# Kernel tuning notes

Measured on AMD Instinct MI355X. Metric: run time of the kernel, lower is better.

Reference implementation:

```python
import jax, jax.numpy as jnp
import numpy as np


def setup_inputs() -> dict:
    key = jax.random.key(0)
    x = jax.random.normal(key, (4096, 16384), dtype=jnp.float32)
    return {"x": x, "k": 64}


def reference(x, k):
    # TopK activation: keep the k largest-|value| entries per row, zero the rest.
    if k <= 0:
        return jnp.zeros_like(x)
    kk = min(k, x.shape[-1])
    _, idx = jax.lax.top_k(jnp.abs(x), kk)          # idx: [rows, kk]
    rows = jnp.arange(x.shape[0])[:, None]          # [rows, 1]
    mask = jnp.zeros_like(x).at[rows, idx].set(1.0)  # scatter ones at top-k positions
    return x * mask
```

## Files before the change

kernel.cpp:

```cpp
#include <hip/hip_runtime.h>

#define ROW_LEN 16384
#define THREADS 256
#define VPT 16
#define NBINS 2048
#define CAP 1024

typedef float f4v __attribute__((ext_vector_type(4)));

__global__ __launch_bounds__(THREADS, 4)
void topk_act_kernel(const float* __restrict__ x, const int* __restrict__ kptr,
                     float* __restrict__ out)
{
    const int t = threadIdx.x;
    const long long row = blockIdx.x;
    const f4v* __restrict__ xv = (const f4v*)(x + row * ROW_LEN);
    f4v* __restrict__ ov = (f4v*)(out + row * ROW_LEN);

    const int k = *kptr;
    if (k <= 0) {
        f4v z = (f4v)(0.0f);
        #pragma unroll
        for (int j = 0; j < VPT; ++j)
            __builtin_nontemporal_store(z, &ov[j * THREADS + t]);
        return;
    }
    const unsigned kk = (unsigned)(k < ROW_LEN ? k : ROW_LEN);

    float va[VPT * 4];
    #pragma unroll
    for (int j = 0; j < VPT; ++j) {
        f4v tmp = __builtin_nontemporal_load(&xv[j * THREADS + t]);
        va[4 * j + 0] = tmp.x;
        va[4 * j + 1] = tmp.y;
        va[4 * j + 2] = tmp.z;
        va[4 * j + 3] = tmp.w;
    }

    __shared__ unsigned hist[NBINS];
    __shared__ unsigned tsum[THREADS];
    __shared__ unsigned long long lst[CAP];
    __shared__ unsigned s_cnt;
    __shared__ int s_b;
    __shared__ unsigned s_g;
    __shared__ unsigned long long s_ccut;

    for (int i = t; i < NBINS; i += THREADS) hist[i] = 0u;
    if (t == 0) s_cnt = 0u;
    __syncthreads();

    #pragma unroll
    for (int e = 0; e < VPT * 4; ++e) {
        float a = fabsf(va[e]);
        int bin = (int)(a * 512.0f);
        bin = bin > (NBINS - 1) ? (NBINS - 1) : bin;
        atomicAdd(&hist[bin], 1u);
    }
    __syncthreads();

    unsigned s = 0;
    #pragma unroll
    for (int i = 0; i < 8; ++i) s += hist[t * 8 + i];
    tsum[t] = s;
    __syncthreads();
    for (int off = 1; off < THREADS; off <<= 1) {
        unsigned add = (t + off < THREADS) ? tsum[t + off] : 0u;
        __syncthreads();
        tsum[t] += add;
        __syncthreads();
    }
    {
        unsigned acc = (t + 1 < THREADS) ? tsum[t + 1] : 0u;
        #pragma unroll
        for (int i = 7; i >= 0; --i) {
            int bin = t * 8 + i;
            unsigned h = hist[bin];
            if (acc < kk && acc + h >= kk) { s_b = bin; s_g = acc; }
            acc += h;
        }
    }
    __syncthreads();

    const int b = s_b;
    const unsigned g = s_g;

    #pragma unroll
    for (int e = 0; e < VPT * 4; ++e) {
        float a = fabsf(va[e]);
        int bin = (int)(a * 512.0f);
        bin = bin > (NBINS - 1) ? (NBINS - 1) : bin;
        if (bin == b) {
            unsigned p = atomicAdd(&s_cnt, 1u);
            if (p < CAP) {
                unsigned idx = (unsigned)((e >> 2) * (THREADS * 4) + t * 4 + (e & 3));
                lst[p] = ((unsigned long long)__float_as_uint(a) << 32)
                       | (unsigned)(~idx);
            }
        }
    }
    __syncthreads();

    const unsigned m = s_cnt < CAP ? s_cnt : CAP;
    unsigned r = kk - g;
    if (r > m) r = m;

    for (unsigned e = t; e < m; e += THREADS) {
        unsigned long long ce = lst[e];
        unsigned rank = 0;
        for (unsigned q = 0; q < m; ++q) rank += (lst[q] > ce) ? 1u : 0u;
        if (rank == r - 1) s_ccut = ce;
    }
    __syncthreads();
    const unsigned long long ccut = s_ccut;

    #pragma unroll
    for (int j = 0; j < VPT; ++j) {
        f4v w;
        #pragma unroll
        for (int c = 0; c < 4; ++c) {
            float f = va[4 * j + c];
            float a = fabsf(f);
            int bin = (int)(a * 512.0f);
            bin = bin > (NBINS - 1) ? (NBINS - 1) : bin;
            bool keep;
            if (bin > b) keep = true;
            else if (bin < b) keep = false;
            else {
                unsigned idx = (unsigned)(j * (THREADS * 4) + t * 4 + c);
                unsigned long long ce = ((unsigned long long)__float_as_uint(a) << 32)
                                      | (unsigned)(~idx);
                keep = (ce >= ccut);
            }
            w[c] = keep ? f : 0.0f;
        }
        __builtin_nontemporal_store(w, &ov[j * THREADS + t]);
    }
}

extern "C" void kernel_launch(void* const* d_in, const int* in_sizes, int n_in,
                              void* d_out, int out_size, void* d_ws, size_t ws_size,
                              hipStream_t stream) {
    const float* x  = (const float*)d_in[0];
    const int*   kp = (const int*)d_in[1];
    float* out = (float*)d_out;
    const int rows = out_size / ROW_LEN;
    topk_act_kernel<<<dim3(rows), dim3(THREADS), 0, stream>>>(x, kp, out);
}
```

Before: 543.6 us.

## Prefilter candidates above fixed threshold, rebin survivors, reload row instead of registers

Stops holding the whole row in registers. It first collects only elements with |x|>=2.0 into shared memory through a wave-ballot compaction. When enough candidates fit, it histograms just those, finds the boundary bin and ranks within that bin. Otherwise it falls back to the full histogram path, which rereads the row from global memory. The final pass reloads x and keeps every element whose key is at or above the cutoff key. This cuts register pressure and per-element shared atomics. The cost is a second global read of each row, and the fixed threshold suits normally distributed inputs.

```diff
diff --git a/kernel.cpp b/kernel.cpp
--- a/kernel.cpp
+++ b/kernel.cpp
@@ -2,17 +2,51 @@
 
 #define ROW_LEN 16384
 #define THREADS 256
-#define VPT 16
+#define ITERS (ROW_LEN / (THREADS * 4))
 #define NBINS 2048
 #define CAP 1024
+#define TPRE 2.0f
 
 typedef float f4v __attribute__((ext_vector_type(4)));
 
-__global__ __launch_bounds__(THREADS, 4)
+__device__ __forceinline__ unsigned long long make_key(float a, unsigned idx) {
+    return ((unsigned long long)__float_as_uint(a) << 32) | (unsigned)(~idx);
+}
+
+__device__ __forceinline__ void find_boundary(const unsigned* hist, unsigned kk,
+                                              int* s_b, unsigned* s_g, unsigned* wtot) {
+    const int t = threadIdx.x;
+    const int lane = t & 63;
+    const int w = t >> 6;
+    unsigned s_own = 0;
+    #pragma unroll
+    for (int i = 0; i < 8; ++i) s_own += hist[t * 8 + i];
+    unsigned acc = s_own;
+    #pragma unroll
+    for (int off = 1; off < 64; off <<= 1) {
+        unsigned v = __shfl_down(acc, off);
+        if (lane + off < 64) acc += v;
+    }
+    if (lane == 0) wtot[w] = acc;
+    __syncthreads();
+    unsigned addw = 0;
+    for (int w2 = w + 1; w2 < 4; ++w2) addw += wtot[w2];
+    unsigned above = acc - s_own + addw;
+    #pragma unroll
+    for (int i = 7; i >= 0; --i) {
+        unsigned h = hist[t * 8 + i];
+        if (above < kk && above + h >= kk) { *s_b = t * 8 + i; *s_g = above; }
+        above += h;
+    }
+    __syncthreads();
+}
+
+__global__ __launch_bounds__(THREADS)
 void topk_act_kernel(const float* __restrict__ x, const int* __restrict__ kptr,
                      float* __restrict__ out)
 {
     const int t = threadIdx.x;
+    const int lane = t & 63;
     const long long row = blockIdx.x;
     const f4v* __restrict__ xv = (const f4v*)(x + row * ROW_LEN);
     f4v* __restrict__ ov = (f4v*)(out + row * ROW_LEN);
@@ -21,119 +55,142 @@
     if (k <= 0) {
         f4v z = (f4v)(0.0f);
         #pragma unroll
-        for (int j = 0; j < VPT; ++j)
+        for (int j = 0; j < ITERS; ++j)
             __builtin_nontemporal_store(z, &ov[j * THREADS + t]);
         return;
     }
     const unsigned kk = (unsigned)(k < ROW_LEN ? k : ROW_LEN);
 
-    float va[VPT * 4];
-    #pragma unroll
-    for (int j = 0; j < VPT; ++j) {
-        f4v tmp = __builtin_nontemporal_load(&xv[j * THREADS + t]);
-        va[4 * j + 0] = tmp.x;
-        va[4 * j + 1] = tmp.y;
-        va[4 * j + 2] = tmp.z;
-        va[4 * j + 3] = tmp.w;
-    }
-
     __shared__ unsigned hist[NBINS];
-    __shared__ unsigned tsum[THREADS];
     __shared__ unsigned long long lst[CAP];
+    __shared__ unsigned wtot[4];
     __shared__ unsigned s_cnt;
     __shared__ int s_b;
     __shared__ unsigned s_g;
     __shared__ unsigned long long s_ccut;
 
-    for (int i = t; i < NBINS; i += THREADS) hist[i] = 0u;
     if (t == 0) s_cnt = 0u;
     __syncthreads();
 
-    #pragma unroll
-    for (int e = 0; e < VPT * 4; ++e) {
-        float a = fabsf(va[e]);
-        int bin = (int)(a * 512.0f);
-        bin = bin > (NBINS - 1) ? (NBINS - 1) : bin;
-        atomicAdd(&hist[bin], 1u);
-    }
-    __syncthreads();
-
-    unsigned s = 0;
-    #pragma unroll
-    for (int i = 0; i < 8; ++i) s += hist[t * 8 + i];
-    tsum[t] = s;
-    __syncthreads();
-    for (int off = 1; off < THREADS; off <<= 1) {
-        unsigned add = (t + off < THREADS) ? tsum[t + off] : 0u;
-        __syncthreads();
-        tsum[t] += add;
-        __syncthreads();
-    }
-    {
-        unsigned acc = (t + 1 < THREADS) ? tsum[t + 1] : 0u;
+    const unsigned long long lmask_lt = (1ull << lane) - 1ull;
+
+    for (int it = 0; it < ITERS; ++it) {
+        f4v v = xv[it * THREADS + t];
         #pragma unroll
-        for (int i = 7; i >= 0; --i) {
-            int bin = t * 8 + i;
-            unsigned h = hist[bin];
-            if (acc < kk && acc + h >= kk) { s_b = bin; s_g = acc; }
-            acc += h;
-        }
-    }
-    __syncthreads();
-
-    const int b = s_b;
-    const unsigned g = s_g;
-
-    #pragma unroll
-    for (int e = 0; e < VPT * 4; ++e) {
-        float a = fabsf(va[e]);
-        int bin = (int)(a * 512.0f);
-        bin = bin > (NBINS - 1) ? (NBINS - 1) : bin;
-        if (bin == b) {
-            unsigned p = atomicAdd(&s_cnt, 1u);
-            if (p < CAP) {
-                unsigned idx = (unsigned)((e >> 2) * (THREADS * 4) + t * 4 + (e & 3));
-                lst[p] = ((unsigned long long)__float_as_uint(a) << 32)
-                       | (unsigned)(~idx);
-            }
-        }
-    }
-    __syncthreads();
-
-    const unsigned m = s_cnt < CAP ? s_cnt : CAP;
-    unsigned r = kk - g;
-    if (r > m) r = m;
-
-    for (unsigned e = t; e < m; e += THREADS) {
-        unsigned long long ce = lst[e];
-        unsigned rank = 0;
-        for (unsigned q = 0; q < m; ++q) rank += (lst[q] > ce) ? 1u : 0u;
-        if (rank == r - 1) s_ccut = ce;
-    }
-    __syncthreads();
+        for (int c = 0; c < 4; ++c) {
+            float a = fabsf(v[c]);
+            bool cond = (a >= TPRE);
+            unsigned long long mk = __ballot(cond);
+            unsigned cnt = (unsigned)__popcll(mk);
+            if (cnt) {
+                unsigned base = 0;
+                if (lane == 0) base = atomicAdd(&s_cnt, cnt);
+                base = __shfl(base, 0);
+                if (cond) {
+                    unsigned pos = base + (unsigned)__popcll(mk & lmask_lt);
+                    if (pos < CAP) {
+                        unsigned idx = (unsigned)((it * THREADS + t) * 4 + c);
+                        lst[pos] = make_key(a, idx);
+                    }
+                }
+            }
+        }
+    }
+    __syncthreads();
+
+    const unsigned m_all = s_cnt;
+    const bool fast = (m_all >= kk && m_all <= CAP);
+
+    if (fast) {
+        for (int i = t; i < NBINS; i += THREADS) hist[i] = 0u;
+        __syncthreads();
+        for (unsigned e = t; e < m_all; e += THREADS) {
+            float a = __uint_as_float((unsigned)(lst[e] >> 32));
+            int rb = (int)((a - TPRE) * 1024.0f);
+            rb = rb > (NBINS - 1) ? (NBINS - 1) : rb;
+            atomicAdd(&hist[rb], 1u);
+        }
+        __syncthreads();
+        find_boundary(hist, kk, &s_b, &s_g, wtot);
+        const int bsel = s_b;
+        const unsigned r = kk - s_g;
+        for (unsigned e = t; e < m_all; e += THREADS) {
+            unsigned long long key = lst[e];
+            float a = __uint_as_float((unsigned)(key >> 32));
+            int rb = (int)((a - TPRE) * 1024.0f);
+            rb = rb > (NBINS - 1) ? (NBINS - 1) : rb;
+            if (rb == bsel) {
+                unsigned rank = 0;
+                for (unsigned q = 0; q < m_all; ++q) {
+                    unsigned long long kq = lst[q];
+                    float aq = __uint_as_float((unsigned)(kq >> 32));
+                    int rbq = (int)((aq - TPRE) * 1024.0f);
+                    rbq = rbq > (NBINS - 1) ? (NBINS - 1) : rbq;
+                    rank += (rbq == bsel && kq > key) ? 1u : 0u;
+                }
+                if (rank == r - 1) s_ccut = key;
+            }
+        }
+        __syncthreads();
+    } else {
+        for (int i = t; i < NBINS; i += THREADS) hist[i] = 0u;
+        __syncthreads();
+        for (int it = 0; it < ITERS; ++it) {
+            f4v v = xv[it * THREADS + t];
+            #pragma unroll
+            for (int c = 0; c < 4; ++c) {
+                float a = fabsf(v[c]);
+                int bin = (int)(a * 512.0f);
+                bin = bin > (NBINS - 1) ? (NBINS - 1) : bin;
+                atomicAdd(&hist[bin], 1u);
+            }
+        }
+        __syncthreads();
+        find_boundary(hist, kk, &s_b, &s_g, wtot);
+        const int b = s_b;
+        const unsigned r = kk - s_g;
+        if (t == 0) s_cnt = 0u;
+        __syncthreads();
+        for (int it = 0; it < ITERS; ++it) {
+            f4v v = xv[it * THREADS + t];
+            #pragma unroll
+            for (int c = 0; c < 4; ++c) {
+                float a = fabsf(v[c]);
+                int bin = (int)(a * 512.0f);
+                bin = bin > (NBINS - 1) ? (NBINS - 1) : bin;
+                if (bin == b) {
+                    unsigned p = atomicAdd(&s_cnt, 1u);
+                    if (p < CAP) {
+                        unsigned idx = (unsigned)((it * THREADS + t) * 4 + c);
+                        lst[p] = make_key(a, idx);
+                    }
+                }
+            }
+        }
+        __syncthreads();
+        const unsigned mb = s_cnt < CAP ? s_cnt : CAP;
+        for (unsigned e = t; e < mb; e += THREADS) {
+            unsigned long long key = lst[e];
+            unsigned rank = 0;
+            for (unsigned q = 0; q < mb; ++q) rank += (lst[q] > key) ? 1u : 0u;
+            if (rank == r - 1) s_ccut = key;
+        }
+        __syncthreads();
+    }
+
     const unsigned long long ccut = s_ccut;
 
-    #pragma unroll
-    for (int j = 0; j < VPT; ++j) {
+    for (int it = 0; it < ITERS; ++it) {
+        f4v v = xv[it * THREADS + t];
         f4v w;
         #pragma unroll
         for (int c = 0; c < 4; ++c) {
-            float f = va[4 * j + c];
-            float a = fabsf(f);
-            int bin = (int)(a * 512.0f);
-            bin = bin > (NBINS - 1) ? (NBINS - 1) : bin;
-            bool keep;
-            if (bin > b) keep = true;
-            else if (bin < b) keep = false;
-            else {
-                unsigned idx = (unsigned)(j * (THREADS * 4) + t * 4 + c);
-                unsigned long long ce = ((unsigned long long)__float_as_uint(a) << 32)
-                                      | (unsigned)(~idx);
-                keep = (ce >= ccut);
-            }
-            w[c] = keep ? f : 0.0f;
-        }
-        __builtin_nontemporal_store(w, &ov[j * THREADS + t]);
+            float f = v[c];
+            unsigned idx = (unsigned)((it * THREADS + t) * 4 + c);
+            unsigned long long key = make_key(fabsf(f), idx);
+            w[c] = (key >= ccut) ? f : 0.0f;
+        }
+        __builtin_nontemporal_store(w, &ov[it * THREADS + t]);
     }
 }
 
```

After: 517.0 us. 1.05x faster.
